# Optimization experiments

Measured on AMD Instinct MI355X. Metric: run time of the kernel, lower is better.

Reference implementation:

```python
import jax, jax.numpy as jnp
import numpy as np

VOCAB = 50257
NUM_TAGS = 50
EMB_DIM = 128
CTX = 2
N_TOKENS = 262144


def setup_inputs() -> dict:
    key = jax.random.key(0)
    k1, k2, k3, k4 = jax.random.split(key, 4)
    tokens = jax.random.randint(k1, (N_TOKENS,), 0, VOCAB, dtype=jnp.int64 if jax.config.jax_enable_x64 else jnp.int32)
    emb_table = jax.random.normal(k2, (VOCAB, EMB_DIM), dtype=jnp.float32)
    W = jax.random.normal(k3, (NUM_TAGS, EMB_DIM * (1 + 2 * CTX)), dtype=jnp.float32) * 0.05
    b = jax.random.normal(k4, (NUM_TAGS,), dtype=jnp.float32) * 0.05
    return {"tokens": tokens, "emb_table": emb_table, "W": W, "b": b}


def reference(tokens, emb_table, W, b):
    # [N, D] embedding gather
    emb = emb_table[tokens]
    n = emb.shape[0]
    # zero-pad CTX positions on each side (matches torch.zeros_like padding)
    padded = jnp.pad(emb, ((CTX, CTX), (0, 0)))
    # sliding window concat: [N, (2*CTX+1)*D] via 2*CTX+1 shifted views
    windows = jnp.concatenate([padded[i:i + n] for i in range(2 * CTX + 1)], axis=-1)
    logits = windows @ W.T + b  # [N, num_tags]
    log_probs = jax.nn.log_softmax(logits, axis=-1)
    return log_probs
```

## Files before the change

### kernel.cpp

```cpp
#include <hip/hip_runtime.h>
#include <hip/hip_bf16.h>

#define VOCAB 50257
#define NTAGS 50
#define EMB   128
#define NTOK  262144
#define KD    640
#define WPAD  64

#define TAGP  64
#define NZ    320
#define ZROWS 50304

#define TOK   64
#define RWS   68
#define CHR   40
#define NCHUNK (RWS*CHR)
#define NITER  ((NCHUNK+63)/64)

typedef __attribute__((ext_vector_type(4))) float f32x4;
typedef __attribute__((ext_vector_type(8))) short bf16x8;

__device__ __forceinline__ ushort f2bf(float f) {
    union { float f; unsigned u; } v; v.f = f;
    unsigned u = v.u;
    return (ushort)((u + 0x7fffu + ((u >> 16) & 1u)) >> 16);
}

__device__ __forceinline__ void gload_lds16(const void* g, void* l) {
    __builtin_amdgcn_global_load_lds(
        (const __attribute__((address_space(1))) unsigned*)g,
        (__attribute__((address_space(3))) unsigned*)l, 16, 0, 0);
}

__global__ void conv2_k(const float* __restrict__ W, const float* __restrict__ b,
                        ushort* __restrict__ Wt, float* __restrict__ biasp) {
    int i = blockIdx.x * blockDim.x + threadIdx.x;
    if (i < NZ * EMB / 4) {
        int j = i * 4;
        int n = j / EMB, d = j % EMB;
        int p = n >> 6, tg = n & 63;
        ushort4 o = {0, 0, 0, 0};
        if (tg < NTAGS) {
            float4 w4 = *(const float4*)(W + tg * KD + p * EMB + d);
            o = { f2bf(w4.x), f2bf(w4.y), f2bf(w4.z), f2bf(w4.w) };
        }
        *(ushort4*)(Wt + j) = o;
    } else {
        int k = i - NZ * EMB / 4;
        if (k < TAGP / 4) {
            #pragma unroll
            for (int e = 0; e < 4; ++e) {
                int j = k * 4 + e;
                biasp[j] = (j < NTAGS) ? b[j] : 0.f;
            }
        }
    }
}

__global__ __launch_bounds__(256)
void zt_k(const float* __restrict__ emb, const ushort* __restrict__ Wt,
          ushort* __restrict__ ZT) {
    __shared__ __align__(16) char wlds[NZ * EMB * 2];

    const int tid  = threadIdx.x;
    const int lane = tid & 63;
    const int wave = tid >> 6;
    const int c = lane & 15, q = lane >> 4;
    const int vb = blockIdx.x * 64;

    #pragma unroll
    for (int it = 0; it < 20; ++it) {
        int g = it * 256 + tid;
        int n = g >> 4, j = g & 15;
        const char* src = (const char*)Wt + n * 256 + ((j ^ (n & 7)) << 4);
        gload_lds16(src, wlds + it * 4096 + wave * 1024);
    }

    const int row = vb + wave * 16 + c;
    const bool ok = row < VOCAB;
    const float* rp = emb + (size_t)(ok ? row : 0) * EMB;
    bf16x8 A[4];
    #pragma unroll
    for (int kk = 0; kk < 4; ++kk) {
        float4 lo = {0,0,0,0}, hi = {0,0,0,0};
        if (ok) {
            lo = *(const float4*)(rp + kk * 32 + q * 8);
            hi = *(const float4*)(rp + kk * 32 + q * 8 + 4);
        }
        bf16x8 a;
        a[0]=(short)f2bf(lo.x); a[1]=(short)f2bf(lo.y);
        a[2]=(short)f2bf(lo.z); a[3]=(short)f2bf(lo.w);
        a[4]=(short)f2bf(hi.x); a[5]=(short)f2bf(hi.y);
        a[6]=(short)f2bf(hi.z); a[7]=(short)f2bf(hi.w);
        A[kk] = a;
    }
    __syncthreads();

    #pragma unroll
    for (int ng = 0; ng < 5; ++ng) {
        bf16x8 B[4][4];
        #pragma unroll
        for (int nt = 0; nt < 4; ++nt) {
            #pragma unroll
            for (int kk = 0; kk < 4; ++kk) {
                int r  = ng * 64 + nt * 16 + c;
                int ph = (kk * 4 + q) ^ (c & 7);
                B[nt][kk] = *(const bf16x8*)(wlds + r * 256 + ph * 16);
            }
        }
        f32x4 acc[4];
        #pragma unroll
        for (int nt = 0; nt < 4; ++nt) acc[nt] = (f32x4){0.f,0.f,0.f,0.f};
        #pragma unroll
        for (int kk = 0; kk < 4; ++kk)
            #pragma unroll
            for (int nt = 0; nt < 4; ++nt)
                acc[nt] = __builtin_amdgcn_mfma_f32_16x16x32_bf16(
                    A[kk], B[nt][kk], acc[nt], 0, 0, 0);
        #pragma unroll
        for (int nt = 0; nt < 4; ++nt)
            #pragma unroll
            for (int j = 0; j < 4; ++j)
                ZT[(size_t)(vb + wave * 16 + q * 4 + j) * NZ + ng * 64 + nt * 16 + c] =
                    f2bf(acc[nt][j]);
    }
}

__global__ __launch_bounds__(64, 3)
void tag_k(const int* __restrict__ tokens, const ushort* __restrict__ ZT,
           const float* __restrict__ biasp, float* __restrict__ out) {
    __shared__ __align__(16) char smem[RWS * 640 + RWS * 4];
    int* ids = (int*)(smem + RWS * 640);

    const int l  = threadIdx.x;
    const int bb = blockIdx.x * TOK;

    {
        int t = bb - 2 + l;
        ids[l] = (t >= 0 && t < NTOK) ? tokens[t] : VOCAB;
        if (l < RWS - 64) {
            int t2 = bb + 62 + l;
            ids[64 + l] = (t2 >= 0 && t2 < NTOK) ? tokens[t2] : VOCAB;
        }
    }
    __syncthreads();

    #pragma unroll
    for (int rd = 0; rd < 4; ++rd) {
        const int w0 = rd * 11;
        const int w1 = (rd == 3) ? NITER : (w0 + 11);
        f32x4 buf[11];
        #pragma unroll
        for (int w = w0; w < w1; ++w) {
            int g = w * 64 + l;
            bool okg = g < NCHUNK;
            int r  = okg ? (g / CHR) : 0;
            int ch = g - r * CHR;
            buf[w - w0] = okg
                ? *(const f32x4*)((const char*)ZT + (size_t)ids[r] * 640 + ch * 16)
                : (f32x4){0.f,0.f,0.f,0.f};
        }
        #pragma unroll
        for (int w = w0; w < w1; ++w) {
            int g = w * 64 + l;
            if (g < NCHUNK) {
                int r  = g / CHR;
                int ch = g - r * CHR;
                int i  = ch & 7, p = ch >> 3;
                *(f32x4*)(smem + r * 640 + p * 128 + ((i ^ (r & 7)) << 4)) = buf[w - w0];
            }
        }
    }
    __syncthreads();

    float acc[56];
    #pragma unroll
    for (int g = 0; g < 14; ++g) {
        float4 b4 = *(const float4*)(biasp + g * 4);
        acc[g*4+0] = b4.x; acc[g*4+1] = b4.y; acc[g*4+2] = b4.z; acc[g*4+3] = b4.w;
    }
    {
        bf16x8 v[5][7];
        #pragma unroll
        for (int p = 0; p < 5; ++p) {
            const int rp = l + p;
            const char* rb = smem + rp * 640;
            const int rx = (rp & 7) << 4;
            #pragma unroll
            for (int j = 0; j < 7; ++j)
                v[p][j] = *(const bf16x8*)(rb + p * 128 + ((j << 4) ^ rx));
        }
        #pragma unroll
        for (int p = 0; p < 5; ++p)
            #pragma unroll
            for (int j = 0; j < 7; ++j)
                #pragma unroll
                for (int e = 0; e < 8; ++e) {
                    unsigned u = (unsigned)(ushort)v[p][j][e] << 16;
                    acc[j*8+e] += __uint_as_float(u);
                }
    }

    float m = acc[0];
    #pragma unroll
    for (int j = 1; j < NTAGS; ++j) m = fmaxf(m, acc[j]);
    float s = 0.f;
    #pragma unroll
    for (int j = 0; j < NTAGS; ++j) s += __expf(acc[j] - m);
    const float L = m + __logf(s);

    __syncthreads();
    #pragma unroll
    for (int k = 0; k < 25; ++k) {
        float2 st = { acc[2*k] - L, acc[2*k+1] - L };
        *(float2*)(smem + (size_t)l * 200 + k * 8) = st;
    }
    __syncthreads();
    char* ob = (char*)out + (size_t)bb * 200;
    #pragma unroll
    for (int w = 0; w < 13; ++w) {
        if (w < 12 || l < 32) {
            f32x4 d = *(const f32x4*)(smem + w * 1024 + (size_t)l * 16);
            *(f32x4*)(ob + w * 1024 + (size_t)l * 16) = d;
        }
    }
}

__global__ void fb_conv_k(const float* __restrict__ emb, const float* __restrict__ W,
                          ushort* __restrict__ embb, ushort* __restrict__ wb) {
    const int etotal = (VOCAB + 1) * EMB;
    int idx = (blockIdx.x * blockDim.x + threadIdx.x) * 4;
    if (idx < etotal) {
        float4 v = {0.f, 0.f, 0.f, 0.f};
        if (idx < VOCAB * EMB) v = *(const float4*)(emb + idx);
        ushort4 o = { f2bf(v.x), f2bf(v.y), f2bf(v.z), f2bf(v.w) };
        *(ushort4*)(embb + idx) = o;
    } else {
        int wi = idx - etotal;
        if (wi < WPAD * KD) {
            #pragma unroll
            for (int k = 0; k < 4; ++k) {
                int j = wi + k;
                int tag = j / KD;
                wb[j] = f2bf(tag < NTAGS ? W[j] : 0.f);
            }
        }
    }
}

__global__ __launch_bounds__(64, 2)
void fb_tag_k(const int* __restrict__ tokens, const ushort* __restrict__ embb,
              const ushort* __restrict__ Wb, const float* __restrict__ bias,
              float* __restrict__ out) {
    __shared__ ushort smem[68 * EMB];
    const int lane = threadIdx.x & 63;
    const int c = lane & 15;
    const int q = lane >> 4;
    const int bb = blockIdx.x * 64;
    const int rsub = lane >> 4;

    int tokid[17];
    #pragma unroll
    for (int g = 0; g < 17; ++g) {
        int t = bb - 2 + g * 4 + rsub;
        tokid[g] = (t >= 0 && t < NTOK) ? tokens[t] : VOCAB;
    }
    const ushort* bp[4];
    #pragma unroll
    for (int nt = 0; nt < 4; ++nt)
        bp[nt] = Wb + (nt * 16 + c) * KD + q * 8;
    bf16x8 Bb[4][4];
    #pragma unroll
    for (int s = 0; s < 4; ++s)
        #pragma unroll
        for (int nt = 0; nt < 4; ++nt)
            Bb[s][nt] = *(const bf16x8*)(bp[nt] + (s >> 2) * 128 + (s & 3) * 32);
    float bv[4];
    #pragma unroll
    for (int nt = 0; nt < 4; ++nt) {
        int tag = nt * 16 + c;
        bv[nt] = bias[tag < NTAGS ? tag : NTAGS - 1];
    }
    {
        const int pc = lane & 15;
        #pragma unroll
        for (int g = 0; g < 17; ++g) {
            int i = g * 4 + rsub;
            int sc = pc ^ (i & 7);
            gload_lds16(embb + (size_t)tokid[g] * EMB + sc * 8, (char*)smem + g * 1024);
        }
    }
    __syncthreads();

    f32x4 acc[4][4];
    #pragma unroll
    for (int mt = 0; mt < 4; ++mt)
        #pragma unroll
        for (int nt = 0; nt < 4; ++nt)
            acc[mt][nt] = (f32x4){0.f, 0.f, 0.f, 0.f};
    bf16x8 Ab[2][4];
    #pragma unroll
    for (int s = 0; s < 2; ++s) {
        int p = s >> 2, kk = s & 3;
        int ch = (4 * kk + q) ^ ((c + p) & 7);
        const char* ab = (const char*)smem + (c + p) * 256 + ch * 16;
        #pragma unroll
        for (int mt = 0; mt < 4; ++mt)
            Ab[s][mt] = *(const bf16x8*)(ab + mt * 4096);
    }
    #pragma unroll
    for (int s = 0; s < 20; ++s) {
        __builtin_amdgcn_s_setprio(1);
        #pragma unroll
        for (int mt = 0; mt < 4; ++mt)
            #pragma unroll
            for (int nt = 0; nt < 4; ++nt)
                acc[mt][nt] = __builtin_amdgcn_mfma_f32_16x16x32_bf16(
                    Ab[s & 1][mt], Bb[s & 3][nt], acc[mt][nt], 0, 0, 0);
        __builtin_amdgcn_s_setprio(0);
        if (s + 4 < 20) {
            const int tt = s + 4, p = tt >> 2, kk = tt & 3;
            #pragma unroll
            for (int nt = 0; nt < 4; ++nt)
                Bb[s & 3][nt] = *(const bf16x8*)(bp[nt] + p * 128 + kk * 32);
        }
        if (s + 2 < 20) {
            const int tt = s + 2, p = tt >> 2, kk = tt & 3;
            int ch = (4 * kk + q) ^ ((c + p) & 7);
            const char* ab = (const char*)smem + (c + p) * 256 + ch * 16;
            #pragma unroll
            for (int mt = 0; mt < 4; ++mt)
                Ab[s & 1][mt] = *(const bf16x8*)(ab + mt * 4096);
        }
    }
    #pragma unroll
    for (int mt = 0; mt < 4; ++mt) {
        #pragma unroll
        for (int j = 0; j < 4; ++j) {
            const int row = bb + mt * 16 + q * 4 + j;
            float x[4];
            float m = -1e30f;
            #pragma unroll
            for (int nt = 0; nt < 4; ++nt) {
                float xv = acc[mt][nt][j] + bv[nt];
                x[nt] = xv;
                if (nt * 16 + c < NTAGS) m = fmaxf(m, xv);
            }
            #pragma unroll
            for (int mask = 8; mask >= 1; mask >>= 1)
                m = fmaxf(m, __shfl_xor(m, mask));
            float s = 0.f;
            #pragma unroll
            for (int nt = 0; nt < 4; ++nt)
                if (nt * 16 + c < NTAGS) s += __expf(x[nt] - m);
            #pragma unroll
            for (int mask = 8; mask >= 1; mask >>= 1)
                s += __shfl_xor(s, mask);
            const float L = m + __logf(s);
            #pragma unroll
            for (int nt = 0; nt < 4; ++nt) {
                int tag = nt * 16 + c;
                if (tag < NTAGS) out[row * NTAGS + tag] = x[nt] - L;
            }
        }
    }
}

extern "C" void kernel_launch(void* const* d_in, const int* in_sizes, int n_in,
                              void* d_out, int out_size, void* d_ws, size_t ws_size,
                              hipStream_t stream) {
    const int*   tokens = (const int*)d_in[0];
    const float* emb    = (const float*)d_in[1];
    const float* W      = (const float*)d_in[2];
    const float* b      = (const float*)d_in[3];
    float* out = (float*)d_out;

    const size_t NEED = 82432ull + (size_t)ZROWS * NZ * 2ull;
    if (ws_size >= NEED) {
        ushort* Wt    = (ushort*)d_ws;
        float*  biasp = (float*)((char*)d_ws + 81920);
        ushort* ZT    = (ushort*)((char*)d_ws + 82432);
        conv2_k<<<41, 256, 0, stream>>>(W, b, Wt, biasp);
        zt_k<<<ZROWS / 64, 256, 0, stream>>>(emb, Wt, ZT);
        tag_k<<<NTOK / TOK, 64, 0, stream>>>(tokens, ZT, biasp, out);
    } else {
        ushort* embb = (ushort*)d_ws;
        ushort* Wb   = embb + (size_t)(VOCAB + 1) * EMB;
        const int etotal = (VOCAB + 1) * EMB;
        const int total4 = (etotal + WPAD * KD) / 4;
        fb_conv_k<<<(total4 + 255) / 256, 256, 0, stream>>>(emb, W, embb, Wb);
        fb_tag_k<<<NTOK / 64, 64, 0, stream>>>(tokens, embb, Wb, b, out);
    }
}
```

Before: 74.84 us.

## Fuse weight conversion into ZT kernel, widen ZT tiles, gather directly to LDS

Removes the separate weight/bias conversion kernel: each ZT block now converts W to bf16 itself while staging it into LDS, and handles 128 vocab rows per block (two M-tiles per wave) to amortise that staging. The tag kernel gathers ZT rows straight into LDS with global_load_lds, which removes the token-id staging and the register round trip. It also shrinks the tile to 56 tokens and reads the bias directly. This saves a launch and a pass through registers, at the cost of redundant W conversion per block, idle lanes in tag_k, and a single-block launch-bounds hint.

```diff
diff --git a/kernel.cpp b/kernel.cpp
--- a/kernel.cpp
+++ b/kernel.cpp
@@ -12,8 +12,8 @@
 #define NZ    320
 #define ZROWS 50304
 
-#define TOK   64
-#define RWS   68
+#define TOK   56
+#define RWS   60
 #define CHR   40
 #define NCHUNK (RWS*CHR)
 #define NITER  ((NCHUNK+63)/64)
@@ -33,33 +33,9 @@
         (__attribute__((address_space(3))) unsigned*)l, 16, 0, 0);
 }
 
-__global__ void conv2_k(const float* __restrict__ W, const float* __restrict__ b,
-                        ushort* __restrict__ Wt, float* __restrict__ biasp) {
-    int i = blockIdx.x * blockDim.x + threadIdx.x;
-    if (i < NZ * EMB / 4) {
-        int j = i * 4;
-        int n = j / EMB, d = j % EMB;
-        int p = n >> 6, tg = n & 63;
-        ushort4 o = {0, 0, 0, 0};
-        if (tg < NTAGS) {
-            float4 w4 = *(const float4*)(W + tg * KD + p * EMB + d);
-            o = { f2bf(w4.x), f2bf(w4.y), f2bf(w4.z), f2bf(w4.w) };
-        }
-        *(ushort4*)(Wt + j) = o;
-    } else {
-        int k = i - NZ * EMB / 4;
-        if (k < TAGP / 4) {
-            #pragma unroll
-            for (int e = 0; e < 4; ++e) {
-                int j = k * 4 + e;
-                biasp[j] = (j < NTAGS) ? b[j] : 0.f;
-            }
-        }
-    }
-}
 
 __global__ __launch_bounds__(256)
-void zt_k(const float* __restrict__ emb, const ushort* __restrict__ Wt,
+void zt_k(const float* __restrict__ emb, const float* __restrict__ W,
           ushort* __restrict__ ZT) {
     __shared__ __align__(16) char wlds[NZ * EMB * 2];
 
@@ -67,33 +43,46 @@
     const int lane = tid & 63;
     const int wave = tid >> 6;
     const int c = lane & 15, q = lane >> 4;
-    const int vb = blockIdx.x * 64;
+    const int vb = blockIdx.x * 128;
 
     #pragma unroll
     for (int it = 0; it < 20; ++it) {
         int g = it * 256 + tid;
         int n = g >> 4, j = g & 15;
-        const char* src = (const char*)Wt + n * 256 + ((j ^ (n & 7)) << 4);
-        gload_lds16(src, wlds + it * 4096 + wave * 1024);
-    }
-
-    const int row = vb + wave * 16 + c;
-    const bool ok = row < VOCAB;
-    const float* rp = emb + (size_t)(ok ? row : 0) * EMB;
-    bf16x8 A[4];
-    #pragma unroll
-    for (int kk = 0; kk < 4; ++kk) {
-        float4 lo = {0,0,0,0}, hi = {0,0,0,0};
-        if (ok) {
-            lo = *(const float4*)(rp + kk * 32 + q * 8);
-            hi = *(const float4*)(rp + kk * 32 + q * 8 + 4);
-        }
-        bf16x8 a;
-        a[0]=(short)f2bf(lo.x); a[1]=(short)f2bf(lo.y);
-        a[2]=(short)f2bf(lo.z); a[3]=(short)f2bf(lo.w);
-        a[4]=(short)f2bf(hi.x); a[5]=(short)f2bf(hi.y);
-        a[6]=(short)f2bf(hi.z); a[7]=(short)f2bf(hi.w);
-        A[kk] = a;
+        int tg = n & 63, p = n >> 6;
+        bf16x8 val = (bf16x8){0,0,0,0,0,0,0,0};
+        if (tg < NTAGS) {
+            const float* wp = W + tg * KD + p * EMB + j * 8;
+            f32x4 lo = *(const f32x4*)wp;
+            f32x4 hi = *(const f32x4*)(wp + 4);
+            val[0]=(short)f2bf(lo[0]); val[1]=(short)f2bf(lo[1]);
+            val[2]=(short)f2bf(lo[2]); val[3]=(short)f2bf(lo[3]);
+            val[4]=(short)f2bf(hi[0]); val[5]=(short)f2bf(hi[1]);
+            val[6]=(short)f2bf(hi[2]); val[7]=(short)f2bf(hi[3]);
+        }
+        *(bf16x8*)(wlds + n * 256 + ((j ^ (n & 7)) << 4)) = val;
+    }
+
+    bf16x8 A[2][4];
+    #pragma unroll
+    for (int mt = 0; mt < 2; ++mt) {
+        int row = vb + wave * 32 + mt * 16 + c;
+        bool ok = row < VOCAB;
+        const float* rp = emb + (size_t)(ok ? row : 0) * EMB;
+        #pragma unroll
+        for (int kk = 0; kk < 4; ++kk) {
+            f32x4 lo = {0,0,0,0}, hi = {0,0,0,0};
+            if (ok) {
+                lo = *(const f32x4*)(rp + kk * 32 + q * 8);
+                hi = *(const f32x4*)(rp + kk * 32 + q * 8 + 4);
+            }
+            bf16x8 a;
+            a[0]=(short)f2bf(lo[0]); a[1]=(short)f2bf(lo[1]);
+            a[2]=(short)f2bf(lo[2]); a[3]=(short)f2bf(lo[3]);
+            a[4]=(short)f2bf(hi[0]); a[5]=(short)f2bf(hi[1]);
+            a[6]=(short)f2bf(hi[2]); a[7]=(short)f2bf(hi[3]);
+            A[mt][kk] = a;
+        }
     }
     __syncthreads();
 
@@ -109,82 +98,67 @@
                 B[nt][kk] = *(const bf16x8*)(wlds + r * 256 + ph * 16);
             }
         }
-        f32x4 acc[4];
-        #pragma unroll
-        for (int nt = 0; nt < 4; ++nt) acc[nt] = (f32x4){0.f,0.f,0.f,0.f};
-        #pragma unroll
-        for (int kk = 0; kk < 4; ++kk)
+        #pragma unroll
+        for (int mt = 0; mt < 2; ++mt) {
+            f32x4 acc[4];
+            #pragma unroll
+            for (int nt = 0; nt < 4; ++nt) acc[nt] = (f32x4){0.f,0.f,0.f,0.f};
+            #pragma unroll
+            for (int kk = 0; kk < 4; ++kk)
+                #pragma unroll
+                for (int nt = 0; nt < 4; ++nt)
+                    acc[nt] = __builtin_amdgcn_mfma_f32_16x16x32_bf16(
+                        A[mt][kk], B[nt][kk], acc[nt], 0, 0, 0);
             #pragma unroll
             for (int nt = 0; nt < 4; ++nt)
-                acc[nt] = __builtin_amdgcn_mfma_f32_16x16x32_bf16(
-                    A[kk], B[nt][kk], acc[nt], 0, 0, 0);
-        #pragma unroll
-        for (int nt = 0; nt < 4; ++nt)
-            #pragma unroll
-            for (int j = 0; j < 4; ++j)
-                ZT[(size_t)(vb + wave * 16 + q * 4 + j) * NZ + ng * 64 + nt * 16 + c] =
-                    f2bf(acc[nt][j]);
-    }
-}
-
-__global__ __launch_bounds__(64, 3)
+                #pragma unroll
+                for (int j = 0; j < 4; ++j)
+                    ZT[(size_t)(vb + wave * 32 + mt * 16 + q * 4 + j) * NZ
+                       + ng * 64 + nt * 16 + c] = f2bf(acc[nt][j]);
+        }
+    }
+}
+
+__global__ __launch_bounds__(64, 1)
 void tag_k(const int* __restrict__ tokens, const ushort* __restrict__ ZT,
-           const float* __restrict__ biasp, float* __restrict__ out) {
-    __shared__ __align__(16) char smem[RWS * 640 + RWS * 4];
-    int* ids = (int*)(smem + RWS * 640);
+           const float* __restrict__ bias, float* __restrict__ out) {
+    __shared__ __align__(16) char smem[RWS * 640];
 
     const int l  = threadIdx.x;
     const int bb = blockIdx.x * TOK;
 
+    #pragma unroll
+    for (int w = 0; w < NITER; ++w) {
+        int g = w * 64 + l;
+        if (g < NCHUNK) {
+            int r  = g / CHR;
+            int ch = g - r * CHR;
+            int i  = ch & 7, p = ch >> 3;
+            int t  = bb - 2 + r;
+            int tok = ((unsigned)t < NTOK) ? tokens[t] : VOCAB;
+            const char* src = (const char*)ZT + (size_t)tok * 640
+                              + p * 128 + ((i ^ (r & 7)) << 4);
+            gload_lds16(src, smem + w * 1024);
+        }
+    }
+    __syncthreads();
+
+    float acc[56];
+    #pragma unroll
+    for (int g = 0; g < 12; ++g) {
+        float4 b4 = *(const float4*)(bias + g * 4);
+        acc[g*4+0] = b4.x; acc[g*4+1] = b4.y; acc[g*4+2] = b4.z; acc[g*4+3] = b4.w;
+    }
+    acc[48] = bias[48]; acc[49] = bias[49];
+    #pragma unroll
+    for (int j = 50; j < 56; ++j) acc[j] = 0.f;
+
     {
-        int t = bb - 2 + l;
-        ids[l] = (t >= 0 && t < NTOK) ? tokens[t] : VOCAB;
-        if (l < RWS - 64) {
-            int t2 = bb + 62 + l;
-            ids[64 + l] = (t2 >= 0 && t2 < NTOK) ? tokens[t2] : VOCAB;
-        }
-    }
-    __syncthreads();
-
-    #pragma unroll
-    for (int rd = 0; rd < 4; ++rd) {
-        const int w0 = rd * 11;
-        const int w1 = (rd == 3) ? NITER : (w0 + 11);
-        f32x4 buf[11];
-        #pragma unroll
-        for (int w = w0; w < w1; ++w) {
-            int g = w * 64 + l;
-            bool okg = g < NCHUNK;
-            int r  = okg ? (g / CHR) : 0;
-            int ch = g - r * CHR;
-            buf[w - w0] = okg
-                ? *(const f32x4*)((const char*)ZT + (size_t)ids[r] * 640 + ch * 16)
-                : (f32x4){0.f,0.f,0.f,0.f};
-        }
-        #pragma unroll
-        for (int w = w0; w < w1; ++w) {
-            int g = w * 64 + l;
-            if (g < NCHUNK) {
-                int r  = g / CHR;
-                int ch = g - r * CHR;
-                int i  = ch & 7, p = ch >> 3;
-                *(f32x4*)(smem + r * 640 + p * 128 + ((i ^ (r & 7)) << 4)) = buf[w - w0];
-            }
-        }
-    }
-    __syncthreads();
-
-    float acc[56];
-    #pragma unroll
-    for (int g = 0; g < 14; ++g) {
-        float4 b4 = *(const float4*)(biasp + g * 4);
-        acc[g*4+0] = b4.x; acc[g*4+1] = b4.y; acc[g*4+2] = b4.z; acc[g*4+3] = b4.w;
-    }
-    {
+        const int le = (l < TOK) ? l : (TOK - 1);
         bf16x8 v[5][7];
         #pragma unroll
         for (int p = 0; p < 5; ++p) {
-            const int rp = l + p;
+            const int rp = le + p;
             const char* rb = smem + rp * 640;
             const int rx = (rp & 7) << 4;
             #pragma unroll
@@ -211,18 +185,23 @@
     const float L = m + __logf(s);
 
     __syncthreads();
-    #pragma unroll
-    for (int k = 0; k < 25; ++k) {
-        float2 st = { acc[2*k] - L, acc[2*k+1] - L };
-        *(float2*)(smem + (size_t)l * 200 + k * 8) = st;
-    }
-    __syncthreads();
+    if (l < TOK) {
+        #pragma unroll
+        for (int k = 0; k < 25; ++k) {
+            float2 st = { acc[2*k] - L, acc[2*k+1] - L };
+            *(float2*)(smem + (size_t)l * 200 + k * 8) = st;
+        }
+    }
+    __syncthreads();
+    const int nvalid = (NTOK - bb < TOK) ? (NTOK - bb) : TOK;
+    const int nbytes = nvalid * 200;
     char* ob = (char*)out + (size_t)bb * 200;
     #pragma unroll
-    for (int w = 0; w < 13; ++w) {
-        if (w < 12 || l < 32) {
-            f32x4 d = *(const f32x4*)(smem + w * 1024 + (size_t)l * 16);
-            *(f32x4*)(ob + w * 1024 + (size_t)l * 16) = d;
+    for (int w = 0; w < 11; ++w) {
+        int off = w * 1024 + l * 16;
+        if (off < nbytes) {
+            f32x4 d = *(const f32x4*)(smem + off);
+            *(f32x4*)(ob + off) = d;
         }
     }
 }
@@ -376,14 +355,11 @@
     const float* b      = (const float*)d_in[3];
     float* out = (float*)d_out;
 
-    const size_t NEED = 82432ull + (size_t)ZROWS * NZ * 2ull;
+    const size_t NEED = (size_t)ZROWS * NZ * 2ull;
     if (ws_size >= NEED) {
-        ushort* Wt    = (ushort*)d_ws;
-        float*  biasp = (float*)((char*)d_ws + 81920);
-        ushort* ZT    = (ushort*)((char*)d_ws + 82432);
-        conv2_k<<<41, 256, 0, stream>>>(W, b, Wt, biasp);
-        zt_k<<<ZROWS / 64, 256, 0, stream>>>(emb, Wt, ZT);
-        tag_k<<<NTOK / TOK, 64, 0, stream>>>(tokens, ZT, biasp, out);
+        ushort* ZT = (ushort*)d_ws;
+        zt_k<<<ZROWS / 128, 256, 0, stream>>>(emb, W, ZT);
+        tag_k<<<(NTOK + TOK - 1) / TOK, 64, 0, stream>>>(tokens, ZT, b, out);
     } else {
         ushort* embb = (ushort*)d_ws;
         ushort* Wb   = embb + (size_t)(VOCAB + 1) * EMB;
```

New measurement: 112.9 us. 1.51x slower.
